# Kernel tuning notes

Hardware: AMD Instinct MI355X
Metric: run time of the kernel (lower is better)

## Reference

```python
import jax, jax.numpy as jnp
import numpy as np

B, S, D, DOUT = 4, 4096, 1024, 1024

def setup_inputs() -> dict:
    key = jax.random.key(0)
    k1, k2 = jax.random.split(key)
    x = jax.random.normal(k1, (B, S, D), dtype=jnp.float32)
    kernel = jax.random.normal(k2, (3, D, DOUT), dtype=jnp.float32) * 0.02
    return {"x": x, "kernel": kernel}

def reference(x, kernel):
    # k, q, v: [B, S, DOUT]  (kernel[0]->k, kernel[1]->q, kernel[2]->v as in source)
    k = jnp.einsum('bsd,de->bse', x, kernel[0])
    q = jnp.einsum('bsd,de->bse', x, kernel[1])
    v = jnp.einsum('bsd,de->bse', x, kernel[2])
    dk = jnp.sqrt(jnp.float32(DOUT))
    scores = jnp.einsum('bqe,bke->bqk', q, k) / dk  # [B, S, S]
    weights = jax.nn.softmax(scores, axis=-1)
    return jnp.einsum('bqk,bke->bqe', weights, v)
```

## Files before the change

kernel.cpp:

```cpp
#include <hip/hip_runtime.h>


typedef unsigned short ushort_t;
typedef __attribute__((ext_vector_type(8))) short     bf16x8;
typedef __attribute__((ext_vector_type(4))) float     f32x4;
typedef __attribute__((ext_vector_type(4))) unsigned int u32x4;
typedef __attribute__((ext_vector_type(4))) unsigned short u16x4;

__device__ __forceinline__ unsigned short f2bf(float f) {
  unsigned u = __float_as_uint(f);
  return (unsigned short)((u + 0x7FFFu + ((u >> 16) & 1u)) >> 16);
}
__device__ __forceinline__ float bf2f(unsigned short h) {
  return __uint_as_float((unsigned)h << 16);
}

#define GLOAD16(gsrc, ldst)                                                        \
  __builtin_amdgcn_global_load_lds(                                                \
      (const __attribute__((address_space(1))) void*)(gsrc),                       \
      (__attribute__((address_space(3))) void*)(ldst), 16, 0, 0)
#define WAITVM(N) asm volatile("s_waitcnt vmcnt(" #N ")" ::: "memory")
#define WAITLGKM0() asm volatile("s_waitcnt lgkmcnt(0)" ::: "memory")
#define SCHED0()  __builtin_amdgcn_sched_barrier(0)
#define BARRIER() __builtin_amdgcn_s_barrier()

__global__ __launch_bounds__(256) void cast_bf16_kernel(const float* __restrict__ in,
                                                        ushort_t* __restrict__ out) {
  long i = (long)blockIdx.x * 256 + threadIdx.x;
  const f32x4* p = (const f32x4*)(in + i * 8);
  f32x4 a = p[0], b = p[1];
  u32x4 o;
  o.x = (unsigned)f2bf(a[0]) | ((unsigned)f2bf(a[1]) << 16);
  o.y = (unsigned)f2bf(a[2]) | ((unsigned)f2bf(a[3]) << 16);
  o.z = (unsigned)f2bf(b[0]) | ((unsigned)f2bf(b[1]) << 16);
  o.w = (unsigned)f2bf(b[2]) | ((unsigned)f2bf(b[3]) << 16);
  ((u32x4*)out)[i] = o;
}

__global__ __launch_bounds__(256) void prep_weights_kernel(const float* __restrict__ kern,
                                                           ushort_t* __restrict__ wk,
                                                           ushort_t* __restrict__ wq,
                                                           ushort_t* __restrict__ wvt) {
  int idx = blockIdx.x * 256 + threadIdx.x;
  wk[idx] = f2bf(kern[idx]);
  wq[idx] = f2bf(kern[1048576 + idx] * 0.03125f);
  int e = idx >> 10, d = idx & 1023;
  wvt[idx] = f2bf(kern[2097152 + d * 1024 + e]);
}

template <int OUT_BF16>
__global__ __launch_bounds__(256) void gemm_bt(const ushort_t* __restrict__ A, long lda, long batchA,
                                               const ushort_t* __restrict__ B, long ldb, long batchB,
                                               void* __restrict__ C, long ldc, long batchC,
                                               int K) {
  __shared__ ushort_t lA[128 * 64];
  __shared__ ushort_t lB[128 * 64];

  const int tid  = threadIdx.x;
  const int lane = tid & 63;
  const int wid  = tid >> 6;
  const int wr   = wid >> 1;
  const int wc   = wid & 1;

  const ushort_t* Ab = A + (long)blockIdx.z * batchA + (long)blockIdx.y * 128 * lda;
  const ushort_t* Bb = B + (long)blockIdx.z * batchB + (long)blockIdx.x * 128 * ldb;

  f32x4 acc[4][4] = {};

  const int nkt = K >> 6;
  for (int kt = 0; kt < nkt; ++kt) {
#pragma unroll
    for (int i = 0; i < 4; ++i) {
      int c = tid + i * 256;
      int row = c >> 3, p = c & 7;
      int sc = p ^ (row & 7);
      GLOAD16(Ab + (long)row * lda + kt * 64 + sc * 8, &lA[c * 8]);
    }
#pragma unroll
    for (int i = 0; i < 4; ++i) {
      int c = tid + i * 256;
      int row = c >> 3, p = c & 7;
      int sc = p ^ (row & 7);
      GLOAD16(Bb + (long)row * ldb + kt * 64 + sc * 8, &lB[c * 8]);
    }
    __syncthreads();

    const int lr = lane & 15, lg = lane >> 4;
#pragma unroll
    for (int kk = 0; kk < 2; ++kk) {
      bf16x8 af[4], bfr[4];
#pragma unroll
      for (int m = 0; m < 4; ++m) {
        int row = wr * 64 + m * 16 + lr;
        int cidx = kk * 4 + lg;
        af[m] = *(const bf16x8*)((const char*)lA + row * 128 + ((cidx ^ (row & 7)) << 4));
      }
#pragma unroll
      for (int n = 0; n < 4; ++n) {
        int row = wc * 64 + n * 16 + lr;
        int cidx = kk * 4 + lg;
        bfr[n] = *(const bf16x8*)((const char*)lB + row * 128 + ((cidx ^ (row & 7)) << 4));
      }
#pragma unroll
      for (int m = 0; m < 4; ++m)
#pragma unroll
        for (int n = 0; n < 4; ++n)
          acc[m][n] = __builtin_amdgcn_mfma_f32_16x16x32_bf16(af[m], bfr[n], acc[m][n], 0, 0, 0);
    }
    __syncthreads();
  }

  const long Crow0 = (long)blockIdx.y * 128 + wr * 64;
  const long Ccol0 = (long)blockIdx.x * 128 + wc * 64;
  float*     Cf = (float*)C + (long)blockIdx.z * batchC;
  ushort_t*  Cb = (ushort_t*)C + (long)blockIdx.z * batchC;
#pragma unroll
  for (int m = 0; m < 4; ++m) {
    long r0 = Crow0 + m * 16 + ((lane >> 4) << 2);
#pragma unroll
    for (int n = 0; n < 4; ++n) {
      long cc = Ccol0 + n * 16 + (lane & 15);
#pragma unroll
      for (int j = 0; j < 4; ++j) {
        float val = acc[m][n][j];
        if (OUT_BF16) Cb[(r0 + j) * ldc + cc] = f2bf(val);
        else          Cf[(r0 + j) * ldc + cc] = val;
      }
    }
  }
}


#define PH0(cb, ob, t1, WN)                         \
  readA(cb, 0); readB(cb, 0);                       \
  if (t1 >= 0) { stageA(ob, t1, 1, 0); stageB(ob, t1, 1, 0); } \
  BARRIER(); WAITVM(WN); WAITLGKM0(); SCHED0();     \
  mfma16(0, 0);                                     \
  BARRIER(); SCHED0();

#define PH1(cb, ob, t1, WN)                         \
  readB(cb, 1);                                     \
  if (t1 >= 0) { stageA(ob, t1, 1, 1); stageB(ob, t1, 1, 1); } \
  BARRIER(); WAITVM(WN); WAITLGKM0(); SCHED0();     \
  mfma16(0, 1);                                     \
  BARRIER(); SCHED0();

#define PH2(cb, t2, WN)                             \
  readA(cb, 1);                                     \
  if (t2 >= 0) { stageA(cb, t2, 0, 0); stageA(cb, t2, 0, 1); } \
  BARRIER(); WAITVM(WN); WAITLGKM0(); SCHED0();     \
  mfma16(1, 0);                                     \
  BARRIER(); SCHED0();

#define PH3(cb, t2, WN)                             \
  if (t2 >= 0) { stageB(cb, t2, 0, 0); stageB(cb, t2, 0, 1); } \
  BARRIER(); WAITVM(WN); SCHED0();                  \
  mfma16(1, 1);                                     \
  BARRIER(); SCHED0();

template <int OUT_BF16>
__global__ __launch_bounds__(512, 1) void gemm256(
    const ushort_t* __restrict__ A, long lda, long batchA,
    const ushort_t* __restrict__ B, long ldb, long batchB,
    void* __restrict__ C, long ldc, long batchC,
    int K, int tx, int ty) {
  __shared__ ushort_t lds[2][2][16384];

  const int nblk = gridDim.x;
  int f = blockIdx.x;
  f = (f & 7) * (nblk >> 3) + (f >> 3);
  const int txy = tx * ty;
  const int bz = f / txy;
  int r = f - bz * txy;
  const int by = r / tx;
  const int bx = r - by * tx;

  const int tid  = threadIdx.x;
  const int lane = tid & 63;
  const int wid  = tid >> 6;
  const int wr   = wid >> 2;
  const int wc   = wid & 3;
  const int lr   = lane & 15, lg = lane >> 4;

  const ushort_t* Ab = A + (long)bz * batchA + (long)by * 256 * lda;
  const ushort_t* Bb = B + (long)bz * batchB + (long)bx * 256 * ldb;

  f32x4 acc[8][4] = {};
  bf16x8 afr[4][2];
  bf16x8 bfr[4][2];

  auto stageA = [&](int buf, int kt, int alpha, int half) {
    int c = half * 512 + tid;
    int r7 = c >> 3;
    int row = ((r7 & 63) | ((r7 & 64) << 1)) + alpha * 64;
    int pch = c & 7;
    int sc = pch ^ (row & 7);
    GLOAD16(Ab + (long)row * lda + (long)kt * 64 + sc * 8,
            &lds[buf][0][row * 64 + pch * 8]);
  };
  auto stageB = [&](int buf, int kt, int beta, int half) {
    int c = half * 512 + tid;
    int r7 = c >> 3;
    int row = ((r7 & 31) | ((r7 & 96) << 1)) + beta * 32;
    int pch = c & 7;
    int sc = pch ^ (row & 7);
    GLOAD16(Bb + (long)row * ldb + (long)kt * 64 + sc * 8,
            &lds[buf][1][row * 64 + pch * 8]);
  };
  auto readA = [&](int buf, int mh) {
#pragma unroll
    for (int mm = 0; mm < 4; ++mm)
#pragma unroll
      for (int kk = 0; kk < 2; ++kk) {
        int row = wr * 128 + (mh * 4 + mm) * 16 + lr;
        afr[mm][kk] = *(const bf16x8*)((const char*)&lds[buf][0][0] + row * 128 +
                                       (((kk * 4 + lg) ^ (row & 7)) << 4));
      }
  };
  auto readB = [&](int buf, int nh) {
#pragma unroll
    for (int nn = 0; nn < 2; ++nn)
#pragma unroll
      for (int kk = 0; kk < 2; ++kk) {
        int row = wc * 64 + (nh * 2 + nn) * 16 + lr;
        bfr[nh * 2 + nn][kk] = *(const bf16x8*)((const char*)&lds[buf][1][0] + row * 128 +
                                                (((kk * 4 + lg) ^ (row & 7)) << 4));
      }
  };
  auto mfma16 = [&](int mh, int nh) {
    __builtin_amdgcn_s_setprio(1);
#pragma unroll
    for (int kk = 0; kk < 2; ++kk)
#pragma unroll
      for (int mm = 0; mm < 4; ++mm)
#pragma unroll
        for (int nn = 0; nn < 2; ++nn)
          acc[mh * 4 + mm][nh * 2 + nn] = __builtin_amdgcn_mfma_f32_16x16x32_bf16(
              afr[mm][kk], bfr[nh * 2 + nn][kk], acc[mh * 4 + mm][nh * 2 + nn], 0, 0, 0);
    __builtin_amdgcn_s_setprio(0);
  };

  const int nkt = K >> 6;
  stageA(0, 0, 0, 0); stageA(0, 0, 0, 1); stageB(0, 0, 0, 0); stageB(0, 0, 0, 1);
  stageA(0, 0, 1, 0); stageA(0, 0, 1, 1); stageB(0, 0, 1, 0); stageB(0, 0, 1, 1);
  stageA(1, 1, 0, 0); stageA(1, 1, 0, 1); stageB(1, 1, 0, 0); stageB(1, 1, 0, 1);
  WAITVM(4);
  BARRIER(); SCHED0();

  for (int t = 0; t < nkt - 2; ++t) {
    const int cb = t & 1, ob = cb ^ 1;
    PH0(cb, ob, t + 1, 6)
    PH1(cb, ob, t + 1, 6)
    PH2(cb, t + 2, 6)
    PH3(cb, t + 2, 6)
  }
  {
    const int t = nkt - 2, cb = t & 1, ob = cb ^ 1;
    PH0(cb, ob, t + 1, 6)
    PH1(cb, ob, t + 1, 6)
    PH2(cb, -1, 6)
    PH3(cb, -1, 4)
  }
  {
    const int cb = (nkt - 1) & 1, ob = cb ^ 1;
    PH0(cb, ob, -1, 0)
    PH1(cb, ob, -1, 0)
    PH2(cb, -1, 0)
    PH3(cb, -1, 0)
  }

  const long Crow0 = (long)by * 256 + wr * 128;
  const long Ccol0 = (long)bx * 256 + wc * 64;
  float*     Cf = (float*)C + (long)bz * batchC;
  ushort_t*  Cb = (ushort_t*)C + (long)bz * batchC;
#pragma unroll
  for (int m = 0; m < 8; ++m) {
    long r0 = Crow0 + m * 16 + ((lane >> 4) << 2);
#pragma unroll
    for (int n = 0; n < 4; ++n) {
      long cc = Ccol0 + n * 16 + (lane & 15);
#pragma unroll
      for (int j = 0; j < 4; ++j) {
        float val = acc[m][n][j];
        if (OUT_BF16) Cb[(r0 + j) * ldc + cc] = f2bf(val);
        else          Cf[(r0 + j) * ldc + cc] = val;
      }
    }
  }
}

__global__ __launch_bounds__(256) void softmax_kernel(float* __restrict__ S,
                                                      ushort_t* __restrict__ P,
                                                      long pstride) {
  float* row = S + (long)blockIdx.x * 4096;
  const int tid = threadIdx.x;
  __shared__ float red[4];

  f32x4 v[4];
#pragma unroll
  for (int i = 0; i < 4; ++i) v[i] = ((const f32x4*)row)[tid + i * 256];

  float m = -1e30f;
#pragma unroll
  for (int i = 0; i < 4; ++i)
#pragma unroll
    for (int j = 0; j < 4; ++j) m = fmaxf(m, v[i][j]);
  for (int o = 32; o; o >>= 1) m = fmaxf(m, __shfl_xor(m, o));
  if ((tid & 63) == 0) red[tid >> 6] = m;
  __syncthreads();
  m = fmaxf(fmaxf(red[0], red[1]), fmaxf(red[2], red[3]));

  float p[16];
  float s = 0.f;
#pragma unroll
  for (int i = 0; i < 4; ++i)
#pragma unroll
    for (int j = 0; j < 4; ++j) {
      float e = __expf(v[i][j] - m);
      p[i * 4 + j] = e;
      s += e;
    }
  for (int o = 32; o; o >>= 1) s += __shfl_xor(s, o);
  __syncthreads();
  if ((tid & 63) == 0) red[tid >> 6] = s;
  __syncthreads();
  s = red[0] + red[1] + red[2] + red[3];
  float inv = 1.0f / s;

  u16x4* prow = (u16x4*)(P + (long)blockIdx.x * pstride);
#pragma unroll
  for (int i = 0; i < 4; ++i) {
    u16x4 o;
    o.x = f2bf(p[i * 4 + 0] * inv);
    o.y = f2bf(p[i * 4 + 1] * inv);
    o.z = f2bf(p[i * 4 + 2] * inv);
    o.w = f2bf(p[i * 4 + 3] * inv);
    prow[tid + i * 256] = o;
  }
}

__global__ __launch_bounds__(256) void softmax_bf16_kernel(ushort_t* __restrict__ S) {
  u16x4* row = (u16x4*)(S + (long)blockIdx.x * 4096);
  const int tid = threadIdx.x;
  __shared__ float red[4];

  float v[16];
#pragma unroll
  for (int i = 0; i < 4; ++i) {
    u16x4 h = row[tid + i * 256];
    v[i * 4 + 0] = bf2f(h.x); v[i * 4 + 1] = bf2f(h.y);
    v[i * 4 + 2] = bf2f(h.z); v[i * 4 + 3] = bf2f(h.w);
  }

  float m = -1e30f;
#pragma unroll
  for (int i = 0; i < 16; ++i) m = fmaxf(m, v[i]);
  for (int o = 32; o; o >>= 1) m = fmaxf(m, __shfl_xor(m, o));
  if ((tid & 63) == 0) red[tid >> 6] = m;
  __syncthreads();
  m = fmaxf(fmaxf(red[0], red[1]), fmaxf(red[2], red[3]));

  float s = 0.f;
#pragma unroll
  for (int i = 0; i < 16; ++i) {
    v[i] = __expf(v[i] - m);
    s += v[i];
  }
  for (int o = 32; o; o >>= 1) s += __shfl_xor(s, o);
  __syncthreads();
  if ((tid & 63) == 0) red[tid >> 6] = s;
  __syncthreads();
  s = red[0] + red[1] + red[2] + red[3];
  float inv = 1.0f / s;

#pragma unroll
  for (int i = 0; i < 4; ++i) {
    u16x4 o;
    o.x = f2bf(v[i * 4 + 0] * inv);
    o.y = f2bf(v[i * 4 + 1] * inv);
    o.z = f2bf(v[i * 4 + 2] * inv);
    o.w = f2bf(v[i * 4 + 3] * inv);
    row[tid + i * 256] = o;
  }
}

extern "C" void kernel_launch(void* const* d_in, const int* in_sizes, int n_in,
                              void* d_out, int out_size, void* d_ws, size_t ws_size,
                              hipStream_t stream) {
  const float* x    = (const float*)d_in[0];
  const float* kern = (const float*)d_in[1];
  float* out = (float*)d_out;

  char* p = (char*)d_ws;
  ushort_t* xbf = (ushort_t*)p; p += 33554432;
  ushort_t* t   = (ushort_t*)p; p += 33554432;
  ushort_t* vT  = (ushort_t*)p; p += 33554432;
  ushort_t* wk  = (ushort_t*)p; p += 2097152;
  ushort_t* wq  = (ushort_t*)p; p += 2097152;
  ushort_t* wvt = (ushort_t*)p; p += 2097152;
  ushort_t* mt  = (ushort_t*)p; p += 2097152;
  size_t fixed = (size_t)(p - (char*)d_ws);

  cast_bf16_kernel<<<8192, 256, 0, stream>>>(x, xbf);
  prep_weights_kernel<<<4096, 256, 0, stream>>>(kern, wk, wq, wvt);
  gemm_bt<1><<<dim3(8, 8, 1), 256, 0, stream>>>(wk, 1024, 0, wq, 1024, 0, mt, 1024, 0, 1024);

  const size_t need4 = fixed + 4ull * 33554432;
  const size_t need2 = fixed + 2ull * 33554432;

  if (ws_size >= need2) {
    ushort_t* Sb = (ushort_t*)p;

    gemm256<1><<<dim3(256), dim3(512), 0, stream>>>(xbf, 1024, 0, mt, 1024, 0,
                                                    t, 1024, 0, 1024, 4, 64);
    gemm256<1><<<dim3(256), dim3(512), 0, stream>>>(wvt, 1024, 0,
                                                    xbf, 1024, 4194304,
                                                    vT, 4096, 4194304, 1024, 16, 4);

    const int nb_at_once = (ws_size >= need4) ? 4 : 2;
    for (int b0 = 0; b0 < 4; b0 += nb_at_once) {
      for (int b = b0; b < b0 + nb_at_once; ++b) {
        gemm256<1><<<dim3(256), dim3(512), 0, stream>>>(
            t + (long)b * 4194304, 1024, 0,
            xbf + (long)b * 4194304, 1024, 0,
            Sb + (long)(b - b0) * 16777216, 4096, 0, 1024, 16, 16);
      }
      softmax_bf16_kernel<<<4096 * nb_at_once, 256, 0, stream>>>(Sb);
      gemm256<0><<<dim3(4 * 16 * nb_at_once), dim3(512), 0, stream>>>(
          Sb, 4096, 16777216,
          vT + (long)b0 * 4194304, 4096, 4194304,
          out + (long)b0 * 4194304, 1024, 4194304, 4096, 4, 16);
    }
  } else {
    float* Sbuf = (float*)p;
    long CR = 4096;
    while (CR > 256 && fixed + (size_t)CR * 4096 * 4 > ws_size) CR >>= 1;

    gemm_bt<1><<<dim3(8, 128, 1), 256, 0, stream>>>(xbf, 1024, 0, mt, 1024, 0, t, 1024, 0, 1024);
    gemm_bt<1><<<dim3(32, 8, 4), 256, 0, stream>>>(wvt, 1024, 0,
                                                   xbf, 1024, 4194304,
                                                   vT, 4096, 4194304, 1024);
    for (int b = 0; b < 4; ++b) {
      const ushort_t* xb  = xbf + (long)b * 4194304;
      const ushort_t* vTb = vT  + (long)b * 4194304;
      for (long c0 = 0; c0 < 4096; c0 += CR) {
        const ushort_t* tb = t + ((long)b * 4096 + c0) * 1024;
        gemm_bt<0><<<dim3(32, CR / 128, 1), 256, 0, stream>>>(tb, 1024, 0, xb, 1024, 0,
                                                              Sbuf, 4096, 0, 1024);
        softmax_kernel<<<CR, 256, 0, stream>>>(Sbuf, (ushort_t*)Sbuf, 8192);
        gemm_bt<0><<<dim3(8, CR / 128, 1), 256, 0, stream>>>((const ushort_t*)Sbuf, 8192, 0,
                                                             vTb, 4096, 0,
                                                             out + ((long)b * 4096 + c0) * 1024, 1024, 0,
                                                             4096);
      }
    }
  }
}
```

Before: 412.2 us.

## Restructure gemm256 pipeline into quarter-tile phases and batch score GEMM launches

The 256x256 GEMM main loop is reorganised into four phases. Each phase reads a quarter of the A fragments while the B fragments are read once per k-tile. The per-phase barrier+vmcnt+lgkmcnt waits before the MFMAs are dropped; a single vmcnt wait remains in the last phase, and MFMAs are issued right after LDS reads so the compiler can overlap them. This cuts A-fragment registers and synchronisation points per k-tile, at the cost of relying on compiler-inserted lgkm waits and fewer explicit barriers. Separately, the per-batch score GEMM launches are merged into one batched launch over the z dimension, which removes launch overhead and gives a larger grid.

```diff
diff --git a/kernel.cpp b/kernel.cpp
--- a/kernel.cpp
+++ b/kernel.cpp
@@ -20,7 +20,6 @@
       (const __attribute__((address_space(1))) void*)(gsrc),                       \
       (__attribute__((address_space(3))) void*)(ldst), 16, 0, 0)
 #define WAITVM(N) asm volatile("s_waitcnt vmcnt(" #N ")" ::: "memory")
-#define WAITLGKM0() asm volatile("s_waitcnt lgkmcnt(0)" ::: "memory")
 #define SCHED0()  __builtin_amdgcn_sched_barrier(0)
 #define BARRIER() __builtin_amdgcn_s_barrier()
 
@@ -131,32 +130,25 @@
 }
 
 
-#define PH0(cb, ob, t1, WN)                         \
-  readA(cb, 0); readB(cb, 0);                       \
-  if (t1 >= 0) { stageA(ob, t1, 1, 0); stageB(ob, t1, 1, 0); } \
-  BARRIER(); WAITVM(WN); WAITLGKM0(); SCHED0();     \
-  mfma16(0, 0);                                     \
-  BARRIER(); SCHED0();
-
-#define PH1(cb, ob, t1, WN)                         \
-  readB(cb, 1);                                     \
-  if (t1 >= 0) { stageA(ob, t1, 1, 1); stageB(ob, t1, 1, 1); } \
-  BARRIER(); WAITVM(WN); WAITLGKM0(); SCHED0();     \
-  mfma16(0, 1);                                     \
-  BARRIER(); SCHED0();
-
-#define PH2(cb, t2, WN)                             \
-  readA(cb, 1);                                     \
-  if (t2 >= 0) { stageA(cb, t2, 0, 0); stageA(cb, t2, 0, 1); } \
-  BARRIER(); WAITVM(WN); WAITLGKM0(); SCHED0();     \
-  mfma16(1, 0);                                     \
-  BARRIER(); SCHED0();
-
-#define PH3(cb, t2, WN)                             \
-  if (t2 >= 0) { stageB(cb, t2, 0, 0); stageB(cb, t2, 0, 1); } \
-  BARRIER(); WAITVM(WN); SCHED0();                  \
-  mfma16(1, 1);                                     \
-  BARRIER(); SCHED0();
+#define PH0(cb, ob, t1, STG)                                     \
+  readAq(cb, 0); readB(cb);                                      \
+  if (STG) { stageA(ob, t1, 1, 0); stageB(ob, t1, 1, 0); }       \
+  mfma16q(0); BARRIER(); SCHED0();
+
+#define PH1(cb, ob, t1, STG)                                     \
+  readAq(cb, 1);                                                 \
+  if (STG) { stageA(ob, t1, 1, 1); stageB(ob, t1, 1, 1); }       \
+  mfma16q(1); BARRIER(); SCHED0();
+
+#define PH2(cb, t2, STG)                                         \
+  readAq(cb, 2);                                                 \
+  if (STG) { stageA(cb, t2, 0, 0); stageA(cb, t2, 0, 1); }       \
+  mfma16q(2); BARRIER(); SCHED0();
+
+#define PH3_W4(cb, t2)                                           \
+  readAq(cb, 3);                                                 \
+  stageB(cb, t2, 0, 0); stageB(cb, t2, 0, 1);                    \
+  WAITVM(4); mfma16q(3); BARRIER(); SCHED0();
 
 template <int OUT_BF16>
 __global__ __launch_bounds__(512, 1) void gemm256(
@@ -186,7 +178,7 @@
   const ushort_t* Bb = B + (long)bz * batchB + (long)bx * 256 * ldb;
 
   f32x4 acc[8][4] = {};
-  bf16x8 afr[4][2];
+  bf16x8 afr[2][2];
   bf16x8 bfr[4][2];
 
   auto stageA = [&](int buf, int kt, int alpha, int half) {
@@ -207,36 +199,36 @@
     GLOAD16(Bb + (long)row * ldb + (long)kt * 64 + sc * 8,
             &lds[buf][1][row * 64 + pch * 8]);
   };
-  auto readA = [&](int buf, int mh) {
-#pragma unroll
-    for (int mm = 0; mm < 4; ++mm)
+  auto readAq = [&](int buf, int q) {
+#pragma unroll
+    for (int mm = 0; mm < 2; ++mm)
 #pragma unroll
       for (int kk = 0; kk < 2; ++kk) {
-        int row = wr * 128 + (mh * 4 + mm) * 16 + lr;
+        int row = wr * 128 + (q * 2 + mm) * 16 + lr;
         afr[mm][kk] = *(const bf16x8*)((const char*)&lds[buf][0][0] + row * 128 +
                                        (((kk * 4 + lg) ^ (row & 7)) << 4));
       }
   };
-  auto readB = [&](int buf, int nh) {
-#pragma unroll
-    for (int nn = 0; nn < 2; ++nn)
+  auto readB = [&](int buf) {
+#pragma unroll
+    for (int nn = 0; nn < 4; ++nn)
 #pragma unroll
       for (int kk = 0; kk < 2; ++kk) {
-        int row = wc * 64 + (nh * 2 + nn) * 16 + lr;
-        bfr[nh * 2 + nn][kk] = *(const bf16x8*)((const char*)&lds[buf][1][0] + row * 128 +
-                                                (((kk * 4 + lg) ^ (row & 7)) << 4));
+        int row = wc * 64 + nn * 16 + lr;
+        bfr[nn][kk] = *(const bf16x8*)((const char*)&lds[buf][1][0] + row * 128 +
+                                       (((kk * 4 + lg) ^ (row & 7)) << 4));
       }
   };
-  auto mfma16 = [&](int mh, int nh) {
+  auto mfma16q = [&](int q) {
     __builtin_amdgcn_s_setprio(1);
 #pragma unroll
     for (int kk = 0; kk < 2; ++kk)
 #pragma unroll
-      for (int mm = 0; mm < 4; ++mm)
-#pragma unroll
-        for (int nn = 0; nn < 2; ++nn)
-          acc[mh * 4 + mm][nh * 2 + nn] = __builtin_amdgcn_mfma_f32_16x16x32_bf16(
-              afr[mm][kk], bfr[nh * 2 + nn][kk], acc[mh * 4 + mm][nh * 2 + nn], 0, 0, 0);
+      for (int nn = 0; nn < 4; ++nn)
+#pragma unroll
+        for (int mm = 0; mm < 2; ++mm)
+          acc[q * 2 + mm][nn] = __builtin_amdgcn_mfma_f32_16x16x32_bf16(
+              afr[mm][kk], bfr[nn][kk], acc[q * 2 + mm][nn], 0, 0, 0);
     __builtin_amdgcn_s_setprio(0);
   };
 
@@ -249,24 +241,27 @@
 
   for (int t = 0; t < nkt - 2; ++t) {
     const int cb = t & 1, ob = cb ^ 1;
-    PH0(cb, ob, t + 1, 6)
-    PH1(cb, ob, t + 1, 6)
-    PH2(cb, t + 2, 6)
-    PH3(cb, t + 2, 6)
+    PH0(cb, ob, t + 1, 1)
+    PH1(cb, ob, t + 1, 1)
+    PH2(cb, t + 2, 1)
+    PH3_W4(cb, t + 2)
   }
   {
     const int t = nkt - 2, cb = t & 1, ob = cb ^ 1;
-    PH0(cb, ob, t + 1, 6)
-    PH1(cb, ob, t + 1, 6)
-    PH2(cb, -1, 6)
-    PH3(cb, -1, 4)
+    PH0(cb, ob, t + 1, 1)
+    PH1(cb, ob, t + 1, 1)
+    PH2(cb, 0, 0)
+    readAq(cb, 3);
+    WAITVM(0);
+    mfma16q(3); BARRIER(); SCHED0();
   }
   {
     const int cb = (nkt - 1) & 1, ob = cb ^ 1;
-    PH0(cb, ob, -1, 0)
-    PH1(cb, ob, -1, 0)
-    PH2(cb, -1, 0)
-    PH3(cb, -1, 0)
+    PH0(cb, ob, 0, 0)
+    PH1(cb, ob, 0, 0)
+    PH2(cb, 0, 0)
+    readAq(cb, 3);
+    mfma16q(3);
   }
 
   const long Crow0 = (long)by * 256 + wr * 128;
@@ -419,12 +414,10 @@
 
     const int nb_at_once = (ws_size >= need4) ? 4 : 2;
     for (int b0 = 0; b0 < 4; b0 += nb_at_once) {
-      for (int b = b0; b < b0 + nb_at_once; ++b) {
-        gemm256<1><<<dim3(256), dim3(512), 0, stream>>>(
-            t + (long)b * 4194304, 1024, 0,
-            xbf + (long)b * 4194304, 1024, 0,
-            Sb + (long)(b - b0) * 16777216, 4096, 0, 1024, 16, 16);
-      }
+      gemm256<1><<<dim3(256 * nb_at_once), dim3(512), 0, stream>>>(
+          t + (long)b0 * 4194304, 1024, 4194304,
+          xbf + (long)b0 * 4194304, 1024, 4194304,
+          Sb, 4096, 16777216, 1024, 16, 16);
       softmax_bf16_kernel<<<4096 * nb_at_once, 256, 0, stream>>>(Sb);
       gemm256<0><<<dim3(4 * 16 * nb_at_once), dim3(512), 0, stream>>>(
           Sb, 4096, 16777216,
```

Result: faster. 391.0 us (-5.1%).
